# Kernel tuning notes

Measured on AMD Instinct MI355X. Metric: run time of the kernel, lower is better.

## Reference

```python
import jax, jax.numpy as jnp
import numpy as np

B, S, D_IN, R = 8, 4096, 2048, 64


def setup_inputs() -> dict:
    key = jax.random.key(0)
    kx, kw = jax.random.split(key)
    x = jax.random.normal(kx, (B, S, D_IN), dtype=jnp.float32)
    weight = jax.random.normal(kw, (B, D_IN, R), dtype=jnp.float32) * 0.02
    return {"x": x, "weight": weight}


def reference(x, weight):
    # Batched per-adapter LoRA matmul: [B,S,D] @ [B,D,R] -> [B,S,R]
    return jnp.einsum('bsd,bdr->bsr', x, weight)
```

## Files before the change

### kernel.cpp

```cpp
#include <hip/hip_runtime.h>
#include <hip/hip_bf16.h>

typedef __attribute__((ext_vector_type(8))) short short8;
typedef __attribute__((ext_vector_type(4))) float f32x4;

static constexpr int Bn = 8, Sn = 4096, Dn = 2048, Rn = 64;
static constexpr int NCHUNK = Dn / 64;
static constexpr int WF_PER_B = NCHUNK * 4096;

__device__ __forceinline__ unsigned short f2bf(float f) {
    unsigned u = __builtin_bit_cast(unsigned, f);
    u += 0x7FFFu + ((u >> 16) & 1u);
    return (unsigned short)(u >> 16);
}

__device__ __forceinline__ short8 cvt8(const float4& a, const float4& b) {
    __hip_bfloat162 p0 = __float22bfloat162_rn(float2{a.x, a.y});
    __hip_bfloat162 p1 = __float22bfloat162_rn(float2{a.z, a.w});
    __hip_bfloat162 p2 = __float22bfloat162_rn(float2{b.x, b.y});
    __hip_bfloat162 p3 = __float22bfloat162_rn(float2{b.z, b.w});
    short8 h;
    h[0] = (short)__builtin_bit_cast(unsigned short, p0.x);
    h[1] = (short)__builtin_bit_cast(unsigned short, p0.y);
    h[2] = (short)__builtin_bit_cast(unsigned short, p1.x);
    h[3] = (short)__builtin_bit_cast(unsigned short, p1.y);
    h[4] = (short)__builtin_bit_cast(unsigned short, p2.x);
    h[5] = (short)__builtin_bit_cast(unsigned short, p2.y);
    h[6] = (short)__builtin_bit_cast(unsigned short, p3.x);
    h[7] = (short)__builtin_bit_cast(unsigned short, p3.y);
    return h;
}

__global__ __launch_bounds__(256) void prep_w(const float* __restrict__ W,
                                              unsigned short* __restrict__ Wf) {
    const int t    = blockIdx.x * 256 + threadIdx.x;
    const int lane = t & 63;
    const int nt   = (t >> 6) & 3;
    const int ks   = (t >> 8) & 1;
    const int c    = (t >> 9) & 31;
    const int b    = t >> 14;
    const int g    = lane >> 4;
    const int r    = nt * 16 + (lane & 15);
    const float* __restrict__ src =
        W + ((size_t)b * Dn + c * 64 + ks * 32 + g * 8) * Rn + r;
    short8 o;
#pragma unroll
    for (int f = 0; f < 8; ++f) o[f] = (short)f2bf(src[(size_t)f * Rn]);
    *reinterpret_cast<short8*>(Wf + (size_t)t * 8) = o;
}

struct ABuf { float4 v0, v1, v2, v3; };

__device__ __forceinline__ void load_a(ABuf& A, const float* p) {
    A.v0 = *reinterpret_cast<const float4*>(p);
    A.v1 = *reinterpret_cast<const float4*>(p + 4);
    A.v2 = *reinterpret_cast<const float4*>(p + 32);
    A.v3 = *reinterpret_cast<const float4*>(p + 36);
}
__device__ __forceinline__ void load_b(short8* Bv, const unsigned short* q) {
#pragma unroll
    for (int i = 0; i < 8; ++i)
        Bv[i] = *reinterpret_cast<const short8*>(q + i * 512);
}
__device__ __forceinline__ void compute_chunk(const ABuf& A, const short8* Bv, f32x4* acc) {
    const short8 h0 = cvt8(A.v0, A.v1);
    const short8 h1 = cvt8(A.v2, A.v3);
#pragma unroll
    for (int nt = 0; nt < 4; ++nt)
        acc[nt] = __builtin_amdgcn_mfma_f32_16x16x32_bf16(h0, Bv[nt], acc[nt], 0, 0, 0);
#pragma unroll
    for (int nt = 0; nt < 4; ++nt)
        acc[nt] = __builtin_amdgcn_mfma_f32_16x16x32_bf16(h1, Bv[4 + nt], acc[nt], 0, 0, 0);
}

__global__ __launch_bounds__(512, 4)
void lora_main_ks(const float* __restrict__ X, const unsigned short* __restrict__ Wf,
                  float* __restrict__ O) {
    __shared__ float red[64 * 64];

    const int blk  = blockIdx.x;
    const int b    = blk >> 6;
    const int m0   = (blk & 63) * 64;
    const int tid  = threadIdx.x;
    const int wid  = tid >> 6;
    const int lane = tid & 63;
    const int l15  = lane & 15;
    const int g    = lane >> 4;
    const int kh   = wid >> 2;
    const int wm   = wid & 3;

    const float* xp = X + (size_t)b * (Sn * Dn)
                        + (size_t)(m0 + wm * 16 + l15) * Dn + kh * (Dn / 2) + g * 8;
    const unsigned short* bp = Wf + (size_t)b * WF_PER_B + kh * (WF_PER_B / 2) + lane * 8;

    f32x4 acc[4];
#pragma unroll
    for (int i = 0; i < 4; ++i) acc[i] = f32x4{0.f, 0.f, 0.f, 0.f};

    ABuf A0, A1;
    short8 Bv[8];
    load_a(A0, xp);

    for (int it = 0; it < 8; ++it) {
        load_a(A1, xp + 64);
        load_b(Bv, bp);
        compute_chunk(A0, Bv, acc);

        const bool last = (it == 7);
        load_a(A0, last ? xp : (xp + 128));
        load_b(Bv, bp + 4096);
        compute_chunk(A1, Bv, acc);

        xp += 128;
        bp += 8192;
    }

    const int r0 = g * 4;
    if (kh == 0) {
#pragma unroll
        for (int nt = 0; nt < 4; ++nt)
#pragma unroll
            for (int r = 0; r < 4; ++r)
                red[(wm * 16 + r0 + r) * 64 + nt * 16 + l15] = acc[nt][r];
    }
    __syncthreads();
    if (kh == 1) {
        float* __restrict__ ob = O + (size_t)b * (Sn * Rn) + (size_t)(m0 + wm * 16) * Rn;
#pragma unroll
        for (int nt = 0; nt < 4; ++nt)
#pragma unroll
            for (int r = 0; r < 4; ++r)
                ob[(size_t)(r0 + r) * Rn + nt * 16 + l15] =
                    acc[nt][r] + red[(wm * 16 + r0 + r) * 64 + nt * 16 + l15];
    }
}

__global__ __launch_bounds__(256, 2)
void batch_lora_fused(const float* __restrict__ X, const float* __restrict__ W,
                      float* __restrict__ O) {
    __shared__ unsigned short wlds[2 * 4 * 64 * 8];
    const int blk  = blockIdx.x;
    const int b    = blk >> 6;
    const int m0   = (blk & 63) * 64;
    const int tid  = threadIdx.x;
    const int wid  = tid >> 6;
    const int lane = tid & 63;
    const int l15  = lane & 15;
    const int g    = lane >> 4;
    const float* __restrict__ xrow = X + (size_t)b * (Sn * Dn)
                                       + (size_t)(m0 + wid * 16 + l15) * Dn + g * 8;
    const float* __restrict__ wb = W + (size_t)b * (Dn * Rn);
    f32x4 acc[4];
#pragma unroll
    for (int i = 0; i < 4; ++i) acc[i] = f32x4{0.f, 0.f, 0.f, 0.f};
    for (int kb = 0; kb < Dn; kb += 64) {
#pragma unroll
        for (int i = 0; i < 4; ++i) {
            const int e  = 4 * (tid + 256 * i);
            const int kk = e >> 6;
            const int cc = e & 63;
            const float4 w4 = *reinterpret_cast<const float4*>(
                wb + (size_t)(kb + kk) * Rn + cc);
            const int ks = kk >> 5;
            const int k5 = kk & 31;
            const int nt = cc >> 4;
            const int f  = k5 & 7;
            const int lw = 16 * (k5 >> 3) + (cc & 15);
            unsigned short* dst = &wlds[((ks * 4 + nt) * 64 + lw) * 8 + f];
            dst[0 * 8] = f2bf(w4.x); dst[1 * 8] = f2bf(w4.y);
            dst[2 * 8] = f2bf(w4.z); dst[3 * 8] = f2bf(w4.w);
        }
        __syncthreads();
#pragma unroll
        for (int ks = 0; ks < 2; ++ks) {
            const float* ap = xrow + kb + ks * 32;
            const float4 a0 = *reinterpret_cast<const float4*>(ap);
            const float4 a1 = *reinterpret_cast<const float4*>(ap + 4);
            const short8 ahi = cvt8(a0, a1);
#pragma unroll
            for (int nt = 0; nt < 4; ++nt) {
                const short8 bhi = *reinterpret_cast<const short8*>(
                    &wlds[((ks * 4 + nt) * 64 + lane) * 8]);
                acc[nt] = __builtin_amdgcn_mfma_f32_16x16x32_bf16(ahi, bhi, acc[nt], 0, 0, 0);
            }
        }
        __syncthreads();
    }
    float* __restrict__ ob = O + (size_t)b * (Sn * Rn) + (size_t)(m0 + wid * 16) * Rn;
    const int r0 = g * 4;
#pragma unroll
    for (int nt = 0; nt < 4; ++nt)
#pragma unroll
        for (int r = 0; r < 4; ++r)
            ob[(size_t)(r0 + r) * Rn + nt * 16 + l15] = acc[nt][r];
}

extern "C" void kernel_launch(void* const* d_in, const int* in_sizes, int n_in,
                              void* d_out, int out_size, void* d_ws, size_t ws_size,
                              hipStream_t stream) {
    const float* x = (const float*)d_in[0];
    const float* w = (const float*)d_in[1];
    float* out = (float*)d_out;
    const size_t wf_bytes = (size_t)Bn * WF_PER_B * sizeof(unsigned short);
    if (ws_size >= wf_bytes) {
        unsigned short* wf = (unsigned short*)d_ws;
        prep_w<<<dim3(512), dim3(256), 0, stream>>>(w, wf);
        lora_main_ks<<<dim3(Bn * (Sn / 64)), dim3(512), 0, stream>>>(x, wf, out);
    } else {
        batch_lora_fused<<<dim3(Bn * (Sn / 64)), dim3(256), 0, stream>>>(x, w, out);
    }
}
```

Before: 63.54 us.

## Stagger K-chunk start per wave and use nontemporal loads for X

```diff
diff --git a/kernel.cpp b/kernel.cpp
--- a/kernel.cpp
+++ b/kernel.cpp
@@ -14,7 +14,7 @@
     return (unsigned short)(u >> 16);
 }
 
-__device__ __forceinline__ short8 cvt8(const float4& a, const float4& b) {
+__device__ __forceinline__ short8 cvt8(const f32x4& a, const f32x4& b) {
     __hip_bfloat162 p0 = __float22bfloat162_rn(float2{a.x, a.y});
     __hip_bfloat162 p1 = __float22bfloat162_rn(float2{a.z, a.w});
     __hip_bfloat162 p2 = __float22bfloat162_rn(float2{b.x, b.y});
@@ -49,13 +49,13 @@
     *reinterpret_cast<short8*>(Wf + (size_t)t * 8) = o;
 }
 
-struct ABuf { float4 v0, v1, v2, v3; };
+struct ABuf { f32x4 v0, v1, v2, v3; };
 
 __device__ __forceinline__ void load_a(ABuf& A, const float* p) {
-    A.v0 = *reinterpret_cast<const float4*>(p);
-    A.v1 = *reinterpret_cast<const float4*>(p + 4);
-    A.v2 = *reinterpret_cast<const float4*>(p + 32);
-    A.v3 = *reinterpret_cast<const float4*>(p + 36);
+    A.v0 = __builtin_nontemporal_load(reinterpret_cast<const f32x4*>(p));
+    A.v1 = __builtin_nontemporal_load(reinterpret_cast<const f32x4*>(p + 4));
+    A.v2 = __builtin_nontemporal_load(reinterpret_cast<const f32x4*>(p + 32));
+    A.v3 = __builtin_nontemporal_load(reinterpret_cast<const f32x4*>(p + 36));
 }
 __device__ __forceinline__ void load_b(short8* Bv, const unsigned short* q) {
 #pragma unroll
@@ -89,30 +89,34 @@
     const int kh   = wid >> 2;
     const int wm   = wid & 3;
 
-    const float* xp = X + (size_t)b * (Sn * Dn)
-                        + (size_t)(m0 + wm * 16 + l15) * Dn + kh * (Dn / 2) + g * 8;
-    const unsigned short* bp = Wf + (size_t)b * WF_PER_B + kh * (WF_PER_B / 2) + lane * 8;
+    const float* xbase = X + (size_t)b * (Sn * Dn)
+                           + (size_t)(m0 + wm * 16 + l15) * Dn + kh * (Dn / 2) + g * 8;
+    const unsigned short* bbase = Wf + (size_t)b * WF_PER_B + kh * (WF_PER_B / 2) + lane * 8;
 
     f32x4 acc[4];
 #pragma unroll
     for (int i = 0; i < 4; ++i) acc[i] = f32x4{0.f, 0.f, 0.f, 0.f};
+
+    int j0 = (blk * 5 + wid * 3) & 15;
 
     ABuf A0, A1;
     short8 Bv[8];
-    load_a(A0, xp);
-
+    load_a(A0, xbase + j0 * 64);
+
+#pragma unroll 1
     for (int it = 0; it < 8; ++it) {
-        load_a(A1, xp + 64);
-        load_b(Bv, bp);
+        const int j1 = (j0 + 1) & 15;
+        const int j2 = (j0 + 2) & 15;
+
+        load_a(A1, xbase + j1 * 64);
+        load_b(Bv, bbase + j0 * 4096);
         compute_chunk(A0, Bv, acc);
 
-        const bool last = (it == 7);
-        load_a(A0, last ? xp : (xp + 128));
-        load_b(Bv, bp + 4096);
+        load_a(A0, xbase + j2 * 64);
+        load_b(Bv, bbase + j1 * 4096);
         compute_chunk(A1, Bv, acc);
 
-        xp += 128;
-        bp += 8192;
+        j0 = j2;
     }
 
     const int r0 = g * 4;
@@ -174,8 +178,8 @@
 #pragma unroll
         for (int ks = 0; ks < 2; ++ks) {
             const float* ap = xrow + kb + ks * 32;
-            const float4 a0 = *reinterpret_cast<const float4*>(ap);
-            const float4 a1 = *reinterpret_cast<const float4*>(ap + 4);
+            const f32x4 a0 = *reinterpret_cast<const f32x4*>(ap);
+            const f32x4 a1 = *reinterpret_cast<const f32x4*>(ap + 4);
             const short8 ahi = cvt8(a0, a1);
 #pragma unroll
             for (int nt = 0; nt < 4; ++nt) {
```

Result: slower. 87.22 us (+37.3%).

## Split K four ways per 16-row tile with LDS reduction across waves

Applied to the files above, without the earlier changes.

```diff
diff --git a/kernel.cpp b/kernel.cpp
--- a/kernel.cpp
+++ b/kernel.cpp
@@ -7,6 +7,7 @@
 static constexpr int Bn = 8, Sn = 4096, Dn = 2048, Rn = 64;
 static constexpr int NCHUNK = Dn / 64;
 static constexpr int WF_PER_B = NCHUNK * 4096;
+static constexpr int QSH = WF_PER_B / 4;
 
 __device__ __forceinline__ unsigned short f2bf(float f) {
     unsigned u = __builtin_bit_cast(unsigned, f);
@@ -14,7 +15,7 @@
     return (unsigned short)(u >> 16);
 }
 
-__device__ __forceinline__ short8 cvt8(const float4& a, const float4& b) {
+__device__ __forceinline__ short8 cvt8(const f32x4& a, const f32x4& b) {
     __hip_bfloat162 p0 = __float22bfloat162_rn(float2{a.x, a.y});
     __hip_bfloat162 p1 = __float22bfloat162_rn(float2{a.z, a.w});
     __hip_bfloat162 p2 = __float22bfloat162_rn(float2{b.x, b.y});
@@ -49,89 +50,102 @@
     *reinterpret_cast<short8*>(Wf + (size_t)t * 8) = o;
 }
 
-struct ABuf { float4 v0, v1, v2, v3; };
+struct ABuf { f32x4 v0, v1, v2, v3; };
 
 __device__ __forceinline__ void load_a(ABuf& A, const float* p) {
-    A.v0 = *reinterpret_cast<const float4*>(p);
-    A.v1 = *reinterpret_cast<const float4*>(p + 4);
-    A.v2 = *reinterpret_cast<const float4*>(p + 32);
-    A.v3 = *reinterpret_cast<const float4*>(p + 36);
-}
-__device__ __forceinline__ void load_b(short8* Bv, const unsigned short* q) {
-#pragma unroll
-    for (int i = 0; i < 8; ++i)
-        Bv[i] = *reinterpret_cast<const short8*>(q + i * 512);
-}
-__device__ __forceinline__ void compute_chunk(const ABuf& A, const short8* Bv, f32x4* acc) {
-    const short8 h0 = cvt8(A.v0, A.v1);
-    const short8 h1 = cvt8(A.v2, A.v3);
-#pragma unroll
-    for (int nt = 0; nt < 4; ++nt)
-        acc[nt] = __builtin_amdgcn_mfma_f32_16x16x32_bf16(h0, Bv[nt], acc[nt], 0, 0, 0);
-#pragma unroll
-    for (int nt = 0; nt < 4; ++nt)
-        acc[nt] = __builtin_amdgcn_mfma_f32_16x16x32_bf16(h1, Bv[4 + nt], acc[nt], 0, 0, 0);
-}
-
-__global__ __launch_bounds__(512, 4)
-void lora_main_ks(const float* __restrict__ X, const unsigned short* __restrict__ Wf,
+    A.v0 = *reinterpret_cast<const f32x4*>(p);
+    A.v1 = *reinterpret_cast<const f32x4*>(p + 4);
+    A.v2 = *reinterpret_cast<const f32x4*>(p + 32);
+    A.v3 = *reinterpret_cast<const f32x4*>(p + 36);
+}
+
+#define LD8(q) (*reinterpret_cast<const short8*>(q))
+
+__device__ __forceinline__ void compute_chunk(const ABuf& A, const unsigned short* bq,
+                                              f32x4* acc) {
+    {
+        const short8 q0 = LD8(bq);
+        const short8 q1 = LD8(bq + 512);
+        const short8 q2 = LD8(bq + 1024);
+        const short8 q3 = LD8(bq + 1536);
+        const short8 h0 = cvt8(A.v0, A.v1);
+        acc[0] = __builtin_amdgcn_mfma_f32_16x16x32_bf16(h0, q0, acc[0], 0, 0, 0);
+        acc[1] = __builtin_amdgcn_mfma_f32_16x16x32_bf16(h0, q1, acc[1], 0, 0, 0);
+        acc[2] = __builtin_amdgcn_mfma_f32_16x16x32_bf16(h0, q2, acc[2], 0, 0, 0);
+        acc[3] = __builtin_amdgcn_mfma_f32_16x16x32_bf16(h0, q3, acc[3], 0, 0, 0);
+    }
+    {
+        const short8 q4 = LD8(bq + 2048);
+        const short8 q5 = LD8(bq + 2560);
+        const short8 q6 = LD8(bq + 3072);
+        const short8 q7 = LD8(bq + 3584);
+        const short8 h1 = cvt8(A.v2, A.v3);
+        acc[0] = __builtin_amdgcn_mfma_f32_16x16x32_bf16(h1, q4, acc[0], 0, 0, 0);
+        acc[1] = __builtin_amdgcn_mfma_f32_16x16x32_bf16(h1, q5, acc[1], 0, 0, 0);
+        acc[2] = __builtin_amdgcn_mfma_f32_16x16x32_bf16(h1, q6, acc[2], 0, 0, 0);
+        acc[3] = __builtin_amdgcn_mfma_f32_16x16x32_bf16(h1, q7, acc[3], 0, 0, 0);
+    }
+}
+
+__global__ __launch_bounds__(256, 5)
+void lora_main_k4(const float* __restrict__ X, const unsigned short* __restrict__ Wf,
                   float* __restrict__ O) {
-    __shared__ float red[64 * 64];
+    __shared__ float red[3 * 16 * 65];
 
     const int blk  = blockIdx.x;
-    const int b    = blk >> 6;
-    const int m0   = (blk & 63) * 64;
+    const int b    = blk >> 8;
+    const int m0   = (blk & 255) * 16;
     const int tid  = threadIdx.x;
     const int wid  = tid >> 6;
     const int lane = tid & 63;
     const int l15  = lane & 15;
     const int g    = lane >> 4;
-    const int kh   = wid >> 2;
-    const int wm   = wid & 3;
 
     const float* xp = X + (size_t)b * (Sn * Dn)
-                        + (size_t)(m0 + wm * 16 + l15) * Dn + kh * (Dn / 2) + g * 8;
-    const unsigned short* bp = Wf + (size_t)b * WF_PER_B + kh * (WF_PER_B / 2) + lane * 8;
+                        + (size_t)(m0 + l15) * Dn + wid * (Dn / 4) + g * 8;
+    const unsigned short* bp = Wf + (size_t)b * WF_PER_B + wid * QSH + lane * 8;
 
     f32x4 acc[4];
 #pragma unroll
     for (int i = 0; i < 4; ++i) acc[i] = f32x4{0.f, 0.f, 0.f, 0.f};
 
     ABuf A0, A1;
-    short8 Bv[8];
     load_a(A0, xp);
 
-    for (int it = 0; it < 8; ++it) {
+    for (int it = 0; it < 4; ++it) {
         load_a(A1, xp + 64);
-        load_b(Bv, bp);
-        compute_chunk(A0, Bv, acc);
-
-        const bool last = (it == 7);
+        compute_chunk(A0, bp, acc);
+
+        const bool last = (it == 3);
         load_a(A0, last ? xp : (xp + 128));
-        load_b(Bv, bp + 4096);
-        compute_chunk(A1, Bv, acc);
+        compute_chunk(A1, bp + 4096, acc);
 
         xp += 128;
         bp += 8192;
     }
 
     const int r0 = g * 4;
-    if (kh == 0) {
+    if (wid != 0) {
+        const int base = (wid - 1) * (16 * 65);
 #pragma unroll
         for (int nt = 0; nt < 4; ++nt)
 #pragma unroll
             for (int r = 0; r < 4; ++r)
-                red[(wm * 16 + r0 + r) * 64 + nt * 16 + l15] = acc[nt][r];
+                red[base + (r0 + r) * 65 + nt * 16 + l15] = acc[nt][r];
     }
     __syncthreads();
-    if (kh == 1) {
-        float* __restrict__ ob = O + (size_t)b * (Sn * Rn) + (size_t)(m0 + wm * 16) * Rn;
-#pragma unroll
-        for (int nt = 0; nt < 4; ++nt)
-#pragma unroll
-            for (int r = 0; r < 4; ++r)
-                ob[(size_t)(r0 + r) * Rn + nt * 16 + l15] =
-                    acc[nt][r] + red[(wm * 16 + r0 + r) * 64 + nt * 16 + l15];
+    if (wid == 0) {
+        float* __restrict__ ob = O + (size_t)b * (Sn * Rn) + (size_t)m0 * Rn;
+#pragma unroll
+        for (int nt = 0; nt < 4; ++nt) {
+#pragma unroll
+            for (int r = 0; r < 4; ++r) {
+                const int li = (r0 + r) * 65 + nt * 16 + l15;
+                const float v = acc[nt][r] + red[li] + red[16 * 65 + li]
+                              + red[2 * 16 * 65 + li];
+                ob[(size_t)(r0 + r) * Rn + nt * 16 + l15] = v;
+            }
+        }
     }
 }
 
@@ -174,8 +188,8 @@
 #pragma unroll
         for (int ks = 0; ks < 2; ++ks) {
             const float* ap = xrow + kb + ks * 32;
-            const float4 a0 = *reinterpret_cast<const float4*>(ap);
-            const float4 a1 = *reinterpret_cast<const float4*>(ap + 4);
+            const f32x4 a0 = *reinterpret_cast<const f32x4*>(ap);
+            const f32x4 a1 = *reinterpret_cast<const f32x4*>(ap + 4);
             const short8 ahi = cvt8(a0, a1);
 #pragma unroll
             for (int nt = 0; nt < 4; ++nt) {
@@ -205,7 +219,7 @@
     if (ws_size >= wf_bytes) {
         unsigned short* wf = (unsigned short*)d_ws;
         prep_w<<<dim3(512), dim3(256), 0, stream>>>(w, wf);
-        lora_main_ks<<<dim3(Bn * (Sn / 64)), dim3(512), 0, stream>>>(x, wf, out);
+        lora_main_k4<<<dim3(Bn * (Sn / 16)), dim3(256), 0, stream>>>(x, wf, out);
     } else {
         batch_lora_fused<<<dim3(Bn * (Sn / 64)), dim3(256), 0, stream>>>(x, w, out);
     }
```

Result: slower. 70.14 us (+10.4%).
